# Performance work log

Hardware: AMD Instinct MI355X
Metric: run time of the kernel (lower is better)

## Reference

```python
import jax, jax.numpy as jnp
import numpy as np

E = 800000
N = 50000
D = 128
SLOPE = 0.2


def setup_inputs() -> dict:
    key = jax.random.key(0)
    ks = jax.random.split(key, 8)
    M = jax.random.normal(ks[0], (E, D), dtype=jnp.float32)
    dest = jax.random.randint(ks[1], (E,), 0, N, dtype=jnp.int32)
    rev_index = jax.random.randint(ks[2], (E,), 0, E, dtype=jnp.int32)
    s = 1.0 / np.sqrt(D)
    W0 = jax.random.uniform(ks[3], (D, D), jnp.float32, -s, s)
    b0 = jax.random.uniform(ks[4], (D,), jnp.float32, -s, s)
    W1 = jax.random.uniform(ks[5], (D, D), jnp.float32, -s, s)
    b1 = jax.random.uniform(ks[6], (D,), jnp.float32, -s, s)
    sa = 1.0 / np.sqrt(D)
    a_w = jax.random.uniform(ks[7], (1, D), jnp.float32, -sa, sa)
    a_b = jnp.zeros((1,), jnp.float32)
    return {"M": M, "dest": dest, "rev_index": rev_index, "dim_size": N,
            "W0": W0, "b0": b0, "W1": W1, "b1": b1, "a_w": a_w, "a_b": a_b}


def reference(M, dest, rev_index, dim_size, W0, b0, W1, b1, a_w, a_b):
    # Z = LeakyReLU(W_0(M) + W_1(M[rev_index]))  -> [E, D]
    Z = jax.nn.leaky_relu(M @ W0.T + b0 + M[rev_index] @ W1.T + b1, negative_slope=SLOPE)
    # scores = a(Z) -> [E, 1]; segment softmax over dest
    s = (Z @ a_w.T + a_b)[:, 0]  # [E]
    smax = jax.ops.segment_max(s, dest, num_segments=dim_size)  # [N]
    e = jnp.exp(s - smax[dest])
    denom = jax.ops.segment_sum(e, dest, num_segments=dim_size)  # [N]
    alpha = (e / denom[dest])[:, None]  # [E, 1]
    out = jax.ops.segment_sum(alpha * M, dest, num_segments=dim_size)  # [N, D]
    return out, alpha
```

## Files before the change

### kernel.cpp

```cpp
#include <hip/hip_runtime.h>
#include <hip/hip_bf16.h>


#define SLOPE 0.2f
constexpr int E = 800000;
constexpr int N = 50000;
constexpr int D = 128;
constexpr int TILE_E = 64;
constexpr int NTILES = E / TILE_E;
constexpr int LDA = 264;
constexpr int MAXDEG = 64;

typedef __attribute__((ext_vector_type(8))) short bf16x8;
typedef __attribute__((ext_vector_type(4))) short short4v;
typedef __attribute__((ext_vector_type(4))) float f32x4;

__device__ __forceinline__ short f2bf(float f) {
    unsigned u = __float_as_uint(f);
    u = (u + 0x7fffu + ((u >> 16) & 1u)) >> 16;
    return (short)u;
}

__global__ void convert_w(const float* __restrict__ W0, const float* __restrict__ W1,
                          short* __restrict__ Wbf) {
    int i = blockIdx.x * blockDim.x + threadIdx.x;
    if (i >= D * 256) return;
    int d = i >> 8, k = i & 255;
    float v = (k < 128) ? W0[d * 128 + k] : W1[d * 128 + (k - 128)];
    Wbf[i] = f2bf(v);
}

__global__ void bucket_build(const int* __restrict__ dest, int* __restrict__ cnt,
                             int* __restrict__ bucket) {
    int e = blockIdx.x * blockDim.x + threadIdx.x;
    if (e >= E) return;
    int n = dest[e];
    int pos = atomicAdd(&cnt[n], 1);
    if (pos < MAXDEG) bucket[n * MAXDEG + pos] = e;
}

__global__ __launch_bounds__(512, 4) void score_kernel(
    const float* __restrict__ M, const int* __restrict__ dest,
    const int* __restrict__ rev, const short* __restrict__ Wbf,
    const float* __restrict__ b0, const float* __restrict__ b1,
    const float* __restrict__ a_w, const float* __restrict__ a_b,
    float* __restrict__ pbuf, float* __restrict__ denom)
{
    __shared__ short Alds[TILE_E * LDA];
    __shared__ float red[4][TILE_E];

    const int t = threadIdx.x;
    const int w = t >> 6;
    const int lane = t & 63;
    const int lo = lane & 15, hi = lane >> 4;
    const int er = (w & 1) * 32;
    const int dr = (w >> 1) * 32;

    bf16x8 b[2][8];
#pragma unroll
    for (int j = 0; j < 2; ++j) {
        int d = dr + j * 16 + lo;
#pragma unroll
        for (int ks = 0; ks < 8; ++ks)
            b[j][ks] = *(const bf16x8*)(Wbf + d * 256 + ks * 32 + hi * 8);
    }
    float bs[2], aw[2];
#pragma unroll
    for (int j = 0; j < 2; ++j) {
        int d = dr + j * 16 + lo;
        bs[j] = b0[d] + b1[d];
        aw[j] = a_w[d];
    }
    const float ab = a_b[0];

    const int c  = t & 31;
    const int r0 = t >> 5;

    for (int tile = blockIdx.x; tile < NTILES; tile += gridDim.x) {
        const int ebase = tile * TILE_E;
        __syncthreads();

#pragma unroll
        for (int pp = 0; pp < 2; ++pp) {
            float4 vs[2], vr[2];
            int rv[2];
#pragma unroll
            for (int q = 0; q < 2; ++q)
                rv[q] = rev[ebase + r0 + (pp * 2 + q) * 16];
#pragma unroll
            for (int q = 0; q < 2; ++q)
                vs[q] = ((const float4*)(M + (size_t)(ebase + r0 + (pp * 2 + q) * 16) * D))[c];
#pragma unroll
            for (int q = 0; q < 2; ++q)
                vr[q] = ((const float4*)(M + (size_t)rv[q] * D))[c];
#pragma unroll
            for (int q = 0; q < 2; ++q) {
                int r = r0 + (pp * 2 + q) * 16;
                short4v s0 = { f2bf(vs[q].x), f2bf(vs[q].y), f2bf(vs[q].z), f2bf(vs[q].w) };
                *(short4v*)(Alds + r * LDA + c * 4) = s0;
                short4v s1 = { f2bf(vr[q].x), f2bf(vr[q].y), f2bf(vr[q].z), f2bf(vr[q].w) };
                *(short4v*)(Alds + r * LDA + 128 + c * 4) = s1;
            }
        }
        __syncthreads();

        f32x4 zero = {0.f, 0.f, 0.f, 0.f};
        f32x4 acc[2][2];
#pragma unroll
        for (int i = 0; i < 2; ++i)
#pragma unroll
            for (int j = 0; j < 2; ++j) acc[i][j] = zero;

#pragma unroll
        for (int ks = 0; ks < 8; ++ks) {
            bf16x8 a[2];
#pragma unroll
            for (int i = 0; i < 2; ++i)
                a[i] = *(const bf16x8*)(Alds + (er + i * 16 + lo) * LDA + ks * 32 + hi * 8);
#pragma unroll
            for (int i = 0; i < 2; ++i)
#pragma unroll
                for (int j = 0; j < 2; ++j)
                    acc[i][j] = __builtin_amdgcn_mfma_f32_16x16x32_bf16(a[i], b[j][ks], acc[i][j], 0, 0, 0);
        }

#pragma unroll
        for (int i = 0; i < 2; ++i) {
#pragma unroll
            for (int r = 0; r < 4; ++r) {
                float v = 0.f;
#pragma unroll
                for (int j = 0; j < 2; ++j) {
                    float x = acc[i][j][r] + bs[j];
                    x = (x > 0.f) ? x : SLOPE * x;
                    v += aw[j] * x;
                }
                v += __shfl_xor(v, 1);
                v += __shfl_xor(v, 2);
                v += __shfl_xor(v, 4);
                v += __shfl_xor(v, 8);
                if (lo == 0) red[w >> 1][er + i * 16 + hi * 4 + r] = v;
            }
        }
        __syncthreads();

        if (t < TILE_E) {
            float s = red[0][t] + red[1][t] + red[2][t] + red[3][t] + ab;
            float p = __expf(s);
            pbuf[ebase + t] = p;
            atomicAdd(&denom[dest[ebase + t]], p);
        }
    }
}

__global__ __launch_bounds__(256) void gather_kernel(
    const float* __restrict__ M, float* __restrict__ alpha,
    const float* __restrict__ denom,
    const int* __restrict__ cnt, const int* __restrict__ bucket,
    float* __restrict__ out)
{
    const int n = blockIdx.x * 4 + (threadIdx.x >> 6);
    const int lane = threadIdx.x & 63;
    int c = cnt[n];
    c = (c > MAXDEG) ? MAXDEG : c;
    const float dn = denom[n];
    int e = 0; float a = 0.f;
    if (lane < c) {
        e = bucket[n * MAXDEG + lane];
        a = alpha[e] / dn;
        alpha[e] = a;
    }
    float2 acc = {0.f, 0.f};
    int i = 0;
    for (; i + 4 <= c; i += 4) {
        int   e0 = __shfl(e, i + 0), e1 = __shfl(e, i + 1),
              e2 = __shfl(e, i + 2), e3 = __shfl(e, i + 3);
        float a0 = __shfl(a, i + 0), a1 = __shfl(a, i + 1),
              a2 = __shfl(a, i + 2), a3 = __shfl(a, i + 3);
        float2 v0 = ((const float2*)(M + (size_t)e0 * D))[lane];
        float2 v1 = ((const float2*)(M + (size_t)e1 * D))[lane];
        float2 v2 = ((const float2*)(M + (size_t)e2 * D))[lane];
        float2 v3 = ((const float2*)(M + (size_t)e3 * D))[lane];
        acc.x = fmaf(a0, v0.x, acc.x); acc.y = fmaf(a0, v0.y, acc.y);
        acc.x = fmaf(a1, v1.x, acc.x); acc.y = fmaf(a1, v1.y, acc.y);
        acc.x = fmaf(a2, v2.x, acc.x); acc.y = fmaf(a2, v2.y, acc.y);
        acc.x = fmaf(a3, v3.x, acc.x); acc.y = fmaf(a3, v3.y, acc.y);
    }
    for (; i < c; ++i) {
        int   ei = __shfl(e, i);
        float ai = __shfl(a, i);
        float2 v = ((const float2*)(M + (size_t)ei * D))[lane];
        acc.x = fmaf(ai, v.x, acc.x);
        acc.y = fmaf(ai, v.y, acc.y);
    }
    ((float2*)(out + (size_t)n * D))[lane] = acc;
}

extern "C" void kernel_launch(void* const* d_in, const int* in_sizes, int n_in,
                              void* d_out, int out_size, void* d_ws, size_t ws_size,
                              hipStream_t stream) {
    const float* M   = (const float*)d_in[0];
    const int*   dst = (const int*)d_in[1];
    const int*   rev = (const int*)d_in[2];
    const float* W0  = (const float*)d_in[4];
    const float* b0  = (const float*)d_in[5];
    const float* W1  = (const float*)d_in[6];
    const float* b1  = (const float*)d_in[7];
    const float* a_w = (const float*)d_in[8];
    const float* a_b = (const float*)d_in[9];

    float* out   = (float*)d_out;
    float* alpha = out + (size_t)N * D;

    float* denom  = (float*)d_ws;
    short* Wbf    = (short*)(denom + N);
    int*   cnt    = (int*)(Wbf + D * 256);
    int*   bucket = cnt + N;

    hipMemsetAsync(denom, 0, (size_t)N * sizeof(float), stream);
    hipMemsetAsync(cnt, 0, (size_t)N * sizeof(int), stream);

    convert_w<<<128, 256, 0, stream>>>(W0, W1, Wbf);
    bucket_build<<<(E + 255) / 256, 256, 0, stream>>>(dst, cnt, bucket);
    score_kernel<<<512, 512, 0, stream>>>(M, dst, rev, Wbf, b0, b1, a_w, a_b, alpha, denom);
    gather_kernel<<<N / 4, 256, 0, stream>>>(M, alpha, denom, cnt, bucket, out);
}
```

Measured before the change: 751.6 us.

## Prefetch next tile in score kernel, fuse bucket build, use readlane in gather

The score kernel now software-pipelines its work. It loads the next tile's M rows and reverse rows into registers while the MFMA for the current tile runs, then writes them to LDS after the reduction. This hides global load latency but raises register pressure. The separate bucket_build kernel is folded into the score kernel's epilogue, which removes one launch and a second pass over dest. The two memsets are merged into one by placing cnt next to denom. In the gather kernel, wave-uniform broadcasts use readlane instead of shfl, which avoids LDS-based permutes.

```diff
diff --git a/kernel.cpp b/kernel.cpp
--- a/kernel.cpp
+++ b/kernel.cpp
@@ -10,6 +10,7 @@
 constexpr int NTILES = E / TILE_E;
 constexpr int LDA = 264;
 constexpr int MAXDEG = 64;
+constexpr int SGRID = 512;
 
 typedef __attribute__((ext_vector_type(8))) short bf16x8;
 typedef __attribute__((ext_vector_type(4))) short short4v;
@@ -30,21 +31,13 @@
     Wbf[i] = f2bf(v);
 }
 
-__global__ void bucket_build(const int* __restrict__ dest, int* __restrict__ cnt,
-                             int* __restrict__ bucket) {
-    int e = blockIdx.x * blockDim.x + threadIdx.x;
-    if (e >= E) return;
-    int n = dest[e];
-    int pos = atomicAdd(&cnt[n], 1);
-    if (pos < MAXDEG) bucket[n * MAXDEG + pos] = e;
-}
-
 __global__ __launch_bounds__(512, 4) void score_kernel(
     const float* __restrict__ M, const int* __restrict__ dest,
     const int* __restrict__ rev, const short* __restrict__ Wbf,
     const float* __restrict__ b0, const float* __restrict__ b1,
     const float* __restrict__ a_w, const float* __restrict__ a_b,
-    float* __restrict__ pbuf, float* __restrict__ denom)
+    float* __restrict__ pbuf, float* __restrict__ denom,
+    int* __restrict__ cnt, int* __restrict__ bucket)
 {
     __shared__ short Alds[TILE_E * LDA];
     __shared__ float red[4][TILE_E];
@@ -76,33 +69,46 @@
     const int c  = t & 31;
     const int r0 = t >> 5;
 
-    for (int tile = blockIdx.x; tile < NTILES; tile += gridDim.x) {
-        const int ebase = tile * TILE_E;
+    float4 vs[4], vr[4];
+
+    {
+        const int eb = blockIdx.x * TILE_E;
+        int rv[4];
+#pragma unroll
+        for (int q = 0; q < 4; ++q) rv[q] = rev[eb + r0 + q * 16];
+#pragma unroll
+        for (int q = 0; q < 4; ++q)
+            vs[q] = ((const float4*)(M + (size_t)(eb + r0 + q * 16) * D))[c];
+#pragma unroll
+        for (int q = 0; q < 4; ++q)
+            vr[q] = ((const float4*)(M + (size_t)rv[q] * D))[c];
+#pragma unroll
+        for (int q = 0; q < 4; ++q) {
+            int r = r0 + q * 16;
+            short4v s0 = { f2bf(vs[q].x), f2bf(vs[q].y), f2bf(vs[q].z), f2bf(vs[q].w) };
+            *(short4v*)(Alds + r * LDA + c * 4) = s0;
+            short4v s1 = { f2bf(vr[q].x), f2bf(vr[q].y), f2bf(vr[q].z), f2bf(vr[q].w) };
+            *(short4v*)(Alds + r * LDA + 128 + c * 4) = s1;
+        }
+    }
+
+    for (int tile = blockIdx.x; tile < NTILES; tile += SGRID) {
+        const int nxt = tile + SGRID;
         __syncthreads();
 
-#pragma unroll
-        for (int pp = 0; pp < 2; ++pp) {
-            float4 vs[2], vr[2];
-            int rv[2];
-#pragma unroll
-            for (int q = 0; q < 2; ++q)
-                rv[q] = rev[ebase + r0 + (pp * 2 + q) * 16];
-#pragma unroll
-            for (int q = 0; q < 2; ++q)
-                vs[q] = ((const float4*)(M + (size_t)(ebase + r0 + (pp * 2 + q) * 16) * D))[c];
-#pragma unroll
-            for (int q = 0; q < 2; ++q)
+        if (nxt < NTILES) {
+            const int eb = nxt * TILE_E;
+            int rv[4];
+#pragma unroll
+            for (int q = 0; q < 4; ++q) rv[q] = rev[eb + r0 + q * 16];
+#pragma unroll
+            for (int q = 0; q < 4; ++q)
+                vs[q] = ((const float4*)(M + (size_t)(eb + r0 + q * 16) * D))[c];
+#pragma unroll
+            for (int q = 0; q < 4; ++q)
                 vr[q] = ((const float4*)(M + (size_t)rv[q] * D))[c];
-#pragma unroll
-            for (int q = 0; q < 2; ++q) {
-                int r = r0 + (pp * 2 + q) * 16;
-                short4v s0 = { f2bf(vs[q].x), f2bf(vs[q].y), f2bf(vs[q].z), f2bf(vs[q].w) };
-                *(short4v*)(Alds + r * LDA + c * 4) = s0;
-                short4v s1 = { f2bf(vr[q].x), f2bf(vr[q].y), f2bf(vr[q].z), f2bf(vr[q].w) };
-                *(short4v*)(Alds + r * LDA + 128 + c * 4) = s1;
-            }
-        }
-        __syncthreads();
+        }
+        __builtin_amdgcn_sched_barrier(0);
 
         f32x4 zero = {0.f, 0.f, 0.f, 0.f};
         f32x4 acc[2][2];
@@ -145,10 +151,25 @@
         __syncthreads();
 
         if (t < TILE_E) {
+            int e = tile * TILE_E + t;
             float s = red[0][t] + red[1][t] + red[2][t] + red[3][t] + ab;
             float p = __expf(s);
-            pbuf[ebase + t] = p;
-            atomicAdd(&denom[dest[ebase + t]], p);
+            pbuf[e] = p;
+            int n = dest[e];
+            atomicAdd(&denom[n], p);
+            int pos = atomicAdd(&cnt[n], 1);
+            if (pos < MAXDEG) bucket[n * MAXDEG + pos] = e;
+        }
+
+        if (nxt < NTILES) {
+#pragma unroll
+            for (int q = 0; q < 4; ++q) {
+                int r = r0 + q * 16;
+                short4v s0 = { f2bf(vs[q].x), f2bf(vs[q].y), f2bf(vs[q].z), f2bf(vs[q].w) };
+                *(short4v*)(Alds + r * LDA + c * 4) = s0;
+                short4v s1 = { f2bf(vr[q].x), f2bf(vr[q].y), f2bf(vr[q].z), f2bf(vr[q].w) };
+                *(short4v*)(Alds + r * LDA + 128 + c * 4) = s1;
+            }
         }
     }
 }
@@ -173,10 +194,14 @@
     float2 acc = {0.f, 0.f};
     int i = 0;
     for (; i + 4 <= c; i += 4) {
-        int   e0 = __shfl(e, i + 0), e1 = __shfl(e, i + 1),
-              e2 = __shfl(e, i + 2), e3 = __shfl(e, i + 3);
-        float a0 = __shfl(a, i + 0), a1 = __shfl(a, i + 1),
-              a2 = __shfl(a, i + 2), a3 = __shfl(a, i + 3);
+        int e0 = __builtin_amdgcn_readlane(e, i + 0);
+        int e1 = __builtin_amdgcn_readlane(e, i + 1);
+        int e2 = __builtin_amdgcn_readlane(e, i + 2);
+        int e3 = __builtin_amdgcn_readlane(e, i + 3);
+        float a0 = __uint_as_float(__builtin_amdgcn_readlane(__float_as_uint(a), i + 0));
+        float a1 = __uint_as_float(__builtin_amdgcn_readlane(__float_as_uint(a), i + 1));
+        float a2 = __uint_as_float(__builtin_amdgcn_readlane(__float_as_uint(a), i + 2));
+        float a3 = __uint_as_float(__builtin_amdgcn_readlane(__float_as_uint(a), i + 3));
         float2 v0 = ((const float2*)(M + (size_t)e0 * D))[lane];
         float2 v1 = ((const float2*)(M + (size_t)e1 * D))[lane];
         float2 v2 = ((const float2*)(M + (size_t)e2 * D))[lane];
@@ -187,8 +212,8 @@
         acc.x = fmaf(a3, v3.x, acc.x); acc.y = fmaf(a3, v3.y, acc.y);
     }
     for (; i < c; ++i) {
-        int   ei = __shfl(e, i);
-        float ai = __shfl(a, i);
+        int   ei = __builtin_amdgcn_readlane(e, i);
+        float ai = __uint_as_float(__builtin_amdgcn_readlane(__float_as_uint(a), i));
         float2 v = ((const float2*)(M + (size_t)ei * D))[lane];
         acc.x = fmaf(ai, v.x, acc.x);
         acc.y = fmaf(ai, v.y, acc.y);
@@ -213,15 +238,14 @@
     float* alpha = out + (size_t)N * D;
 
     float* denom  = (float*)d_ws;
-    short* Wbf    = (short*)(denom + N);
-    int*   cnt    = (int*)(Wbf + D * 256);
-    int*   bucket = cnt + N;
-
-    hipMemsetAsync(denom, 0, (size_t)N * sizeof(float), stream);
-    hipMemsetAsync(cnt, 0, (size_t)N * sizeof(int), stream);
+    int*   cnt    = (int*)(denom + N);
+    short* Wbf    = (short*)(cnt + N);
+    int*   bucket = (int*)(Wbf + D * 256);
+
+    hipMemsetAsync(denom, 0, (size_t)2 * N * sizeof(float), stream);
 
     convert_w<<<128, 256, 0, stream>>>(W0, W1, Wbf);
-    bucket_build<<<(E + 255) / 256, 256, 0, stream>>>(dst, cnt, bucket);
-    score_kernel<<<512, 512, 0, stream>>>(M, dst, rev, Wbf, b0, b1, a_w, a_b, alpha, denom);
+    score_kernel<<<SGRID, 512, 0, stream>>>(M, dst, rev, Wbf, b0, b1, a_w, a_b,
+                                            alpha, denom, cnt, bucket);
     gather_kernel<<<N / 4, 256, 0, stream>>>(M, alpha, denom, cnt, bucket, out);
 }
```

After: 772.1 us. +2.7%, slower.

## Pre-convert M to fp16 once and use fp16 MFMA and fp16 gathers

Applied to the files above, without the earlier changes.

Adds a pass that converts M to an fp16 copy in workspace. The score kernel then loads half-width rows and uses f16 MFMA instead of converting to bf16 in-kernel, and the gather kernel also reads the fp16 copy. This is meant to halve bytes on the random row gathers and remove in-loop conversion, at the cost of an extra full read/write pass over M. The final weighted sum over M now uses fp16-rounded inputs, which lowers output precision. Shuffles in the gather loop are replaced with readlane.

```diff
diff --git a/kernel.cpp b/kernel.cpp
--- a/kernel.cpp
+++ b/kernel.cpp
@@ -1,5 +1,4 @@
 #include <hip/hip_runtime.h>
-#include <hip/hip_bf16.h>
 
 
 #define SLOPE 0.2f
@@ -10,24 +9,31 @@
 constexpr int NTILES = E / TILE_E;
 constexpr int LDA = 264;
 constexpr int MAXDEG = 64;
-
-typedef __attribute__((ext_vector_type(8))) short bf16x8;
-typedef __attribute__((ext_vector_type(4))) short short4v;
+constexpr int SGRID = 512;
+
+typedef __attribute__((ext_vector_type(8))) _Float16 f16x8;
+typedef __attribute__((ext_vector_type(4))) _Float16 f16x4;
+typedef __attribute__((ext_vector_type(2))) _Float16 f16x2;
 typedef __attribute__((ext_vector_type(4))) float f32x4;
 
-__device__ __forceinline__ short f2bf(float f) {
-    unsigned u = __float_as_uint(f);
-    u = (u + 0x7fffu + ((u >> 16) & 1u)) >> 16;
-    return (short)u;
-}
-
 __global__ void convert_w(const float* __restrict__ W0, const float* __restrict__ W1,
-                          short* __restrict__ Wbf) {
+                          _Float16* __restrict__ Wh) {
     int i = blockIdx.x * blockDim.x + threadIdx.x;
     if (i >= D * 256) return;
     int d = i >> 8, k = i & 255;
     float v = (k < 128) ? W0[d * 128 + k] : W1[d * 128 + (k - 128)];
-    Wbf[i] = f2bf(v);
+    Wh[i] = (_Float16)v;
+}
+
+__global__ __launch_bounds__(256) void convert_m(const float* __restrict__ M,
+                                                 _Float16* __restrict__ Mh) {
+    const int total = E * D / 4;
+    for (int u = blockIdx.x * blockDim.x + threadIdx.x; u < total;
+         u += gridDim.x * blockDim.x) {
+        float4 v = ((const float4*)M)[u];
+        f16x4 h = { (_Float16)v.x, (_Float16)v.y, (_Float16)v.z, (_Float16)v.w };
+        ((f16x4*)Mh)[u] = h;
+    }
 }
 
 __global__ void bucket_build(const int* __restrict__ dest, int* __restrict__ cnt,
@@ -40,13 +46,13 @@
 }
 
 __global__ __launch_bounds__(512, 4) void score_kernel(
-    const float* __restrict__ M, const int* __restrict__ dest,
-    const int* __restrict__ rev, const short* __restrict__ Wbf,
+    const _Float16* __restrict__ Mh, const int* __restrict__ dest,
+    const int* __restrict__ rev, const _Float16* __restrict__ Wh,
     const float* __restrict__ b0, const float* __restrict__ b1,
     const float* __restrict__ a_w, const float* __restrict__ a_b,
     float* __restrict__ pbuf, float* __restrict__ denom)
 {
-    __shared__ short Alds[TILE_E * LDA];
+    __shared__ _Float16 Alds[TILE_E * LDA];
     __shared__ float red[4][TILE_E];
 
     const int t = threadIdx.x;
@@ -56,13 +62,13 @@
     const int er = (w & 1) * 32;
     const int dr = (w >> 1) * 32;
 
-    bf16x8 b[2][8];
+    f16x8 b[2][8];
 #pragma unroll
     for (int j = 0; j < 2; ++j) {
         int d = dr + j * 16 + lo;
 #pragma unroll
         for (int ks = 0; ks < 8; ++ks)
-            b[j][ks] = *(const bf16x8*)(Wbf + d * 256 + ks * 32 + hi * 8);
+            b[j][ks] = *(const f16x8*)(Wh + d * 256 + ks * 32 + hi * 8);
     }
     float bs[2], aw[2];
 #pragma unroll
@@ -73,34 +79,21 @@
     }
     const float ab = a_b[0];
 
-    const int c  = t & 31;
-    const int r0 = t >> 5;
-
-    for (int tile = blockIdx.x; tile < NTILES; tile += gridDim.x) {
-        const int ebase = tile * TILE_E;
+    const int c16 = t & 15;
+    const int r16 = t >> 4;
+
+    for (int tile = blockIdx.x; tile < NTILES; tile += SGRID) {
+        const int eb = tile * TILE_E;
         __syncthreads();
 
 #pragma unroll
-        for (int pp = 0; pp < 2; ++pp) {
-            float4 vs[2], vr[2];
-            int rv[2];
-#pragma unroll
-            for (int q = 0; q < 2; ++q)
-                rv[q] = rev[ebase + r0 + (pp * 2 + q) * 16];
-#pragma unroll
-            for (int q = 0; q < 2; ++q)
-                vs[q] = ((const float4*)(M + (size_t)(ebase + r0 + (pp * 2 + q) * 16) * D))[c];
-#pragma unroll
-            for (int q = 0; q < 2; ++q)
-                vr[q] = ((const float4*)(M + (size_t)rv[q] * D))[c];
-#pragma unroll
-            for (int q = 0; q < 2; ++q) {
-                int r = r0 + (pp * 2 + q) * 16;
-                short4v s0 = { f2bf(vs[q].x), f2bf(vs[q].y), f2bf(vs[q].z), f2bf(vs[q].w) };
-                *(short4v*)(Alds + r * LDA + c * 4) = s0;
-                short4v s1 = { f2bf(vr[q].x), f2bf(vr[q].y), f2bf(vr[q].z), f2bf(vr[q].w) };
-                *(short4v*)(Alds + r * LDA + 128 + c * 4) = s1;
-            }
+        for (int q = 0; q < 2; ++q) {
+            int r = r16 + q * 32;
+            int rv = rev[eb + r];
+            f16x8 hs = ((const f16x8*)(Mh + (size_t)(eb + r) * D))[c16];
+            f16x8 hr = ((const f16x8*)(Mh + (size_t)rv * D))[c16];
+            *(f16x8*)(Alds + r * LDA + c16 * 8) = hs;
+            *(f16x8*)(Alds + r * LDA + 128 + c16 * 8) = hr;
         }
         __syncthreads();
 
@@ -113,15 +106,15 @@
 
 #pragma unroll
         for (int ks = 0; ks < 8; ++ks) {
-            bf16x8 a[2];
+            f16x8 a[2];
 #pragma unroll
             for (int i = 0; i < 2; ++i)
-                a[i] = *(const bf16x8*)(Alds + (er + i * 16 + lo) * LDA + ks * 32 + hi * 8);
+                a[i] = *(const f16x8*)(Alds + (er + i * 16 + lo) * LDA + ks * 32 + hi * 8);
 #pragma unroll
             for (int i = 0; i < 2; ++i)
 #pragma unroll
                 for (int j = 0; j < 2; ++j)
-                    acc[i][j] = __builtin_amdgcn_mfma_f32_16x16x32_bf16(a[i], b[j][ks], acc[i][j], 0, 0, 0);
+                    acc[i][j] = __builtin_amdgcn_mfma_f32_16x16x32_f16(a[i], b[j][ks], acc[i][j], 0, 0, 0);
         }
 
 #pragma unroll
@@ -145,16 +138,17 @@
         __syncthreads();
 
         if (t < TILE_E) {
+            int e = eb + t;
             float s = red[0][t] + red[1][t] + red[2][t] + red[3][t] + ab;
             float p = __expf(s);
-            pbuf[ebase + t] = p;
-            atomicAdd(&denom[dest[ebase + t]], p);
+            pbuf[e] = p;
+            atomicAdd(&denom[dest[e]], p);
         }
     }
 }
 
 __global__ __launch_bounds__(256) void gather_kernel(
-    const float* __restrict__ M, float* __restrict__ alpha,
+    const _Float16* __restrict__ Mh, float* __restrict__ alpha,
     const float* __restrict__ denom,
     const int* __restrict__ cnt, const int* __restrict__ bucket,
     float* __restrict__ out)
@@ -173,25 +167,29 @@
     float2 acc = {0.f, 0.f};
     int i = 0;
     for (; i + 4 <= c; i += 4) {
-        int   e0 = __shfl(e, i + 0), e1 = __shfl(e, i + 1),
-              e2 = __shfl(e, i + 2), e3 = __shfl(e, i + 3);
-        float a0 = __shfl(a, i + 0), a1 = __shfl(a, i + 1),
-              a2 = __shfl(a, i + 2), a3 = __shfl(a, i + 3);
-        float2 v0 = ((const float2*)(M + (size_t)e0 * D))[lane];
-        float2 v1 = ((const float2*)(M + (size_t)e1 * D))[lane];
-        float2 v2 = ((const float2*)(M + (size_t)e2 * D))[lane];
-        float2 v3 = ((const float2*)(M + (size_t)e3 * D))[lane];
-        acc.x = fmaf(a0, v0.x, acc.x); acc.y = fmaf(a0, v0.y, acc.y);
-        acc.x = fmaf(a1, v1.x, acc.x); acc.y = fmaf(a1, v1.y, acc.y);
-        acc.x = fmaf(a2, v2.x, acc.x); acc.y = fmaf(a2, v2.y, acc.y);
-        acc.x = fmaf(a3, v3.x, acc.x); acc.y = fmaf(a3, v3.y, acc.y);
+        int e0 = __builtin_amdgcn_readlane(e, i + 0);
+        int e1 = __builtin_amdgcn_readlane(e, i + 1);
+        int e2 = __builtin_amdgcn_readlane(e, i + 2);
+        int e3 = __builtin_amdgcn_readlane(e, i + 3);
+        float a0 = __uint_as_float(__builtin_amdgcn_readlane(__float_as_uint(a), i + 0));
+        float a1 = __uint_as_float(__builtin_amdgcn_readlane(__float_as_uint(a), i + 1));
+        float a2 = __uint_as_float(__builtin_amdgcn_readlane(__float_as_uint(a), i + 2));
+        float a3 = __uint_as_float(__builtin_amdgcn_readlane(__float_as_uint(a), i + 3));
+        f16x2 v0 = ((const f16x2*)(Mh + (size_t)e0 * D))[lane];
+        f16x2 v1 = ((const f16x2*)(Mh + (size_t)e1 * D))[lane];
+        f16x2 v2 = ((const f16x2*)(Mh + (size_t)e2 * D))[lane];
+        f16x2 v3 = ((const f16x2*)(Mh + (size_t)e3 * D))[lane];
+        acc.x = fmaf(a0, (float)v0.x, acc.x); acc.y = fmaf(a0, (float)v0.y, acc.y);
+        acc.x = fmaf(a1, (float)v1.x, acc.x); acc.y = fmaf(a1, (float)v1.y, acc.y);
+        acc.x = fmaf(a2, (float)v2.x, acc.x); acc.y = fmaf(a2, (float)v2.y, acc.y);
+        acc.x = fmaf(a3, (float)v3.x, acc.x); acc.y = fmaf(a3, (float)v3.y, acc.y);
     }
     for (; i < c; ++i) {
-        int   ei = __shfl(e, i);
-        float ai = __shfl(a, i);
-        float2 v = ((const float2*)(M + (size_t)ei * D))[lane];
-        acc.x = fmaf(ai, v.x, acc.x);
-        acc.y = fmaf(ai, v.y, acc.y);
+        int   ei = __builtin_amdgcn_readlane(e, i);
+        float ai = __uint_as_float(__builtin_amdgcn_readlane(__float_as_uint(a), i));
+        f16x2 v = ((const f16x2*)(Mh + (size_t)ei * D))[lane];
+        acc.x = fmaf(ai, (float)v.x, acc.x);
+        acc.y = fmaf(ai, (float)v.y, acc.y);
     }
     ((float2*)(out + (size_t)n * D))[lane] = acc;
 }
@@ -212,16 +210,18 @@
     float* out   = (float*)d_out;
     float* alpha = out + (size_t)N * D;
 
-    float* denom  = (float*)d_ws;
-    short* Wbf    = (short*)(denom + N);
-    int*   cnt    = (int*)(Wbf + D * 256);
-    int*   bucket = cnt + N;
-
-    hipMemsetAsync(denom, 0, (size_t)N * sizeof(float), stream);
-    hipMemsetAsync(cnt, 0, (size_t)N * sizeof(int), stream);
-
-    convert_w<<<128, 256, 0, stream>>>(W0, W1, Wbf);
+    float*     denom  = (float*)d_ws;
+    int*       cnt    = (int*)(denom + N);
+    _Float16*  Wh     = (_Float16*)(cnt + N);
+    _Float16*  Mh     = Wh + D * 256;
+    int*       bucket = (int*)(Mh + (size_t)E * D);
+
+    hipMemsetAsync(denom, 0, (size_t)2 * N * sizeof(float), stream);
+
+    convert_w<<<128, 256, 0, stream>>>(W0, W1, Wh);
+    convert_m<<<4096, 256, 0, stream>>>(M, Mh);
     bucket_build<<<(E + 255) / 256, 256, 0, stream>>>(dst, cnt, bucket);
-    score_kernel<<<512, 512, 0, stream>>>(M, dst, rev, Wbf, b0, b1, a_w, a_b, alpha, denom);
-    gather_kernel<<<N / 4, 256, 0, stream>>>(M, alpha, denom, cnt, bucket, out);
-}
+    score_kernel<<<SGRID, 512, 0, stream>>>(Mh, dst, rev, Wh, b0, b1, a_w, a_b,
+                                            alpha, denom);
+    gather_kernel<<<N / 4, 256, 0, stream>>>(Mh, alpha, denom, cnt, bucket, out);
+}
```

Measured after the change: 800.1 us. 1.06x slower.
